# Kernel tuning notes

Measured on AMD Instinct MI355X. Metric: run time of the kernel, lower is better.

The kernel has to match this reference:

```python
import jax, jax.numpy as jnp
import numpy as np

B, N, D, E = 4, 2048, 1024, 4
H = 4 * D  # expert hidden (mult=4)


def setup_inputs() -> dict:
    key = jax.random.key(0)
    ks = jax.random.split(key, 8)
    std = 0.02
    return {
        "x": jax.random.normal(ks[0], (B, N, D), jnp.float32),
        "W_slot": jax.random.normal(ks[1], (E * D, D), jnp.float32) * std,
        "u_slot": jax.random.normal(ks[2], (D,), jnp.float32),
        "sigma_slot": jnp.ones((1,), jnp.float32),
        "W1": jax.random.normal(ks[3], (E, H, D), jnp.float32) * std,
        "b1": jnp.zeros((E, H), jnp.float32),
        "u1": jax.random.normal(ks[4], (E, D), jnp.float32),
        "sig1": jnp.ones((E,), jnp.float32),
        "W2": jax.random.normal(ks[5], (E, D, H), jnp.float32) * std,
        "b2": jnp.zeros((E, D), jnp.float32),
        "u2": jax.random.normal(ks[6], (E, H), jnp.float32),
        "sig2": jnp.ones((E,), jnp.float32),
    }


def _sn_weight(W, u, sigma):
    # One power-iteration step (no_grad in torch -> stop_gradient), then
    # sigma_spec = v^T W u'; weight = W / sigma_spec * learnable sigma.
    v = W @ u
    v = jax.lax.stop_gradient(v / jnp.linalg.norm(v))
    u2 = W.T @ v
    u2 = jax.lax.stop_gradient(u2 / jnp.linalg.norm(u2))
    s = jnp.einsum('c,cd,d->', v, W, u2)
    return W * (sigma / s)


def reference(x, W_slot, u_slot, sigma_slot, W1, b1, u1, sig1, W2, b2, u2, sig2):
    b, n, d = x.shape
    e = W1.shape[0]
    s = n // e  # slots per expert; n divisible by e -> no padding, no mask

    # dynamic slot embeddings from consecutive-segment means
    Wsl = _sn_weight(W_slot, u_slot, sigma_slot[0])          # [e*d, d]
    xm = x.reshape(b, s, e, d).mean(axis=2)                   # [b, s, d]
    slot_embeds = (xm @ Wsl.T).reshape(b, s, e, d)
    slot_embeds = slot_embeds.transpose(0, 2, 1, 3)           # [b, e, s, d]

    logits = jnp.einsum('bnd,besd->bnes', x, slot_embeds)     # [b, n, e, s]
    dispatch = jax.nn.softmax(logits, axis=1)                 # softmax over n
    combine = jax.nn.softmax(logits.reshape(b, n, e * s), axis=-1)

    slots = jnp.einsum('bnd,bnes->ebsd', x, dispatch)         # [e, b, s, d]

    # per-expert FFN with spectral-normed weights (vectorized over experts)
    W1n = jax.vmap(_sn_weight)(W1, u1, sig1)                  # [e, H, d]
    W2n = jax.vmap(_sn_weight)(W2, u2, sig2)                  # [e, d, H]
    h = jax.nn.gelu(jnp.einsum('ebsd,ehd->ebsh', slots, W1n) + b1[:, None, None, :],
                    approximate=False)
    y = jnp.einsum('ebsh,edh->ebsd', h, W2n) + b2[:, None, None, :]

    out = y.transpose(1, 0, 2, 3).reshape(b, e * s, d)        # [b, e*s, d]
    return jnp.einsum('bsd,bns->bnd', out, combine)           # [b, n, d]
```

## Files before the change

kernel.cpp:

```cpp
#include <hip/hip_runtime.h>
#include <hip/hip_bf16.h>
#include <math.h>

constexpr int CB  = 4;
constexpr int CN  = 2048;
constexpr int CD  = 1024;
constexpr int CE  = 4;
constexpr int CS  = 512;
constexpr int CH  = 4096;
constexpr int CES = 2048;

typedef unsigned short u16;
typedef unsigned int   u32;
typedef __bf16 bf16x8 __attribute__((ext_vector_type(8)));
typedef float  f32x4  __attribute__((ext_vector_type(4)));

__device__ __forceinline__ u16 f2bf(float x) {
  u32 u = __float_as_uint(x);
  u = (u + 0x7FFF + ((u >> 16) & 1)) >> 16;
  return (u16)u;
}

__device__ __forceinline__ void gl2lds16(const void* g, void* l) {
  __builtin_amdgcn_global_load_lds(
      (const __attribute__((address_space(1))) void*)g,
      (__attribute__((address_space(3))) void*)l, 16, 0, 0);
}


__global__ __launch_bounds__(256) void gemv_rows_k(const float* __restrict__ W,
    const float* __restrict__ u, float* __restrict__ t1, int M, int K, int ustride) {
  int bi = blockIdx.y;
  int row = blockIdx.x * 4 + (threadIdx.x >> 6);
  int lane = threadIdx.x & 63;
  const float* Wr = W + ((long)bi * M + row) * K;
  const float* ub = u + (long)bi * ustride;
  float s = 0.f;
  for (int k = lane; k < K; k += 64) s += Wr[k] * ub[k];
#pragma unroll
  for (int off = 32; off; off >>= 1) s += __shfl_down(s, off, 64);
  if (lane == 0) t1[bi * M + row] = s;
}

__global__ __launch_bounds__(256) void gemv_cols_k(const float* __restrict__ W,
    const float* __restrict__ t1, float* __restrict__ t2, int M, int K) {
  int bi = blockIdx.z;
  int k = blockIdx.x * 256 + threadIdx.x;
  int m0 = blockIdx.y * 256;
  const float* Wb = W + (long)bi * M * K;
  const float* tb = t1 + bi * M;
  float s = 0.f;
#pragma unroll 4
  for (int m = 0; m < 256; m++) s += Wb[(long)(m0 + m) * K + k] * tb[m0 + m];
  atomicAdd(&t2[bi * K + k], s);
}

__global__ __launch_bounds__(256) void scale_k(const float* __restrict__ t1,
    const float* __restrict__ t2, const float* __restrict__ sig,
    float* __restrict__ out, int M, int K) {
  int bi = blockIdx.x;
  int tid = threadIdx.x;
  __shared__ float red[256];
  float s1 = 0.f;
  for (int i = tid; i < M; i += 256) { float v = t1[bi * M + i]; s1 += v * v; }
  red[tid] = s1; __syncthreads();
  for (int w = 128; w; w >>= 1) { if (tid < w) red[tid] += red[tid + w]; __syncthreads(); }
  float n1 = red[0]; __syncthreads();
  float s2 = 0.f;
  for (int i = tid; i < K; i += 256) { float v = t2[bi * K + i]; s2 += v * v; }
  red[tid] = s2; __syncthreads();
  for (int w = 128; w; w >>= 1) { if (tid < w) red[tid] += red[tid + w]; __syncthreads(); }
  if (tid == 0) out[bi] = sig[bi] * sqrtf(n1 / red[0]);
}

__global__ __launch_bounds__(256) void xm_split_k(const float* __restrict__ x,
    u16* __restrict__ hi, u16* __restrict__ lo) {
  int idx = blockIdx.x * 256 + threadIdx.x;
  int d  = idx & (CD - 1);
  int si = (idx >> 10) & (CS - 1);
  int b  = idx >> 19;
  const float* xp = x + ((long)(b * CN + si * 4)) * CD + d;
  float v = 0.25f * (xp[0] + xp[CD] + xp[2 * CD] + xp[3 * CD]);
  u16 h = f2bf(v);
  hi[idx] = h;
  lo[idx] = f2bf(v - __uint_as_float((u32)h << 16));
}

__global__ __launch_bounds__(256) void split_k(const float* __restrict__ in,
    u16* __restrict__ hi, u16* __restrict__ lo) {
  long i = ((long)blockIdx.x * 256 + threadIdx.x) * 8;
  float4 a = *(const float4*)(in + i);
  float4 b = *(const float4*)(in + i + 4);
  float v[8] = {a.x, a.y, a.z, a.w, b.x, b.y, b.z, b.w};
  u16 oh[8], ol[8];
#pragma unroll
  for (int c = 0; c < 8; c++) {
    u16 h = f2bf(v[c]);
    oh[c] = h;
    ol[c] = f2bf(v[c] - __uint_as_float((u32)h << 16));
  }
  *(uint4*)(hi + i) = *(const uint4*)oh;
  *(uint4*)(lo + i) = *(const uint4*)ol;
}

__global__ __launch_bounds__(256) void colstat_part_k(const float* __restrict__ lg,
    float* __restrict__ pmax, float* __restrict__ psum) {
  int es = blockIdx.x * 256 + threadIdx.x;
  int sl = blockIdx.y;
  int b  = blockIdx.z;
  const float* p = lg + ((long)(b * CN + sl * 256)) * CES + es;
  float m = -1e30f, s = 0.f;
  for (int i = 0; i < 256; i++) {
    float v = p[(long)i * CES];
    if (v > m) { s *= __expf(m - v); m = v; }
    s += __expf(v - m);
  }
  int o = (b * 8 + sl) * CES + es;
  pmax[o] = m; psum[o] = s;
}

__global__ __launch_bounds__(256) void colstat_comb_k(const float* __restrict__ pmax,
    const float* __restrict__ psum, float* __restrict__ cmax, float* __restrict__ csum) {
  int idx = blockIdx.x * 256 + threadIdx.x;
  int b = idx >> 11;
  int es = idx & (CES - 1);
  float m = -1e30f;
#pragma unroll
  for (int sl = 0; sl < 8; sl++) m = fmaxf(m, pmax[(b * 8 + sl) * CES + es]);
  float s = 0.f;
#pragma unroll
  for (int sl = 0; sl < 8; sl++)
    s += psum[(b * 8 + sl) * CES + es] * __expf(pmax[(b * 8 + sl) * CES + es] - m);
  cmax[idx] = m; csum[idx] = s;
}

__global__ __launch_bounds__(256) void rowstat_k(const float* __restrict__ lg,
    float* __restrict__ rmax, float* __restrict__ rsum) {
  int gw = (blockIdx.x * 256 + threadIdx.x) >> 6;
  int lane = threadIdx.x & 63;
  const float* p = lg + (long)gw * CES + lane;
  float v[32];
#pragma unroll
  for (int i = 0; i < 32; i++) v[i] = p[i * 64];
  float m = -1e30f;
#pragma unroll
  for (int i = 0; i < 32; i++) m = fmaxf(m, v[i]);
#pragma unroll
  for (int off = 32; off; off >>= 1) m = fmaxf(m, __shfl_xor(m, off, 64));
  float s = 0.f;
#pragma unroll
  for (int i = 0; i < 32; i++) s += __expf(v[i] - m);
#pragma unroll
  for (int off = 32; off; off >>= 1) s += __shfl_xor(s, off, 64);
  if (lane == 0) { rmax[gw] = m; rsum[gw] = s; }
}

__global__ __launch_bounds__(256) void cvt_bf16_k(const float* __restrict__ in,
                                                  u16* __restrict__ out) {
  long i = ((long)blockIdx.x * 256 + threadIdx.x) * 8;
  float4 a = *(const float4*)(in + i);
  float4 b = *(const float4*)(in + i + 4);
  u16 o[8] = {f2bf(a.x), f2bf(a.y), f2bf(a.z), f2bf(a.w),
              f2bf(b.x), f2bf(b.y), f2bf(b.z), f2bf(b.w)};
  *(uint4*)(out + i) = *(const uint4*)o;
}

__global__ __launch_bounds__(256) void tr_f2b_k(const float* __restrict__ in,
    u16* __restrict__ out, const float* __restrict__ sub, int R, int C, int expmode) {
  __shared__ u16 t[32][33];
  int z = blockIdx.z;
  long ibase = (long)z * R * C;
  int r0 = blockIdx.y * 32, c0 = blockIdx.x * 32;
  int tx = threadIdx.x & 31, ty = threadIdx.x >> 5;
  float cm = expmode ? sub[(long)z * C + c0 + tx] : 0.f;
  for (int rr = ty; rr < 32; rr += 8) {
    float v = in[ibase + (long)(r0 + rr) * C + c0 + tx];
    if (expmode) v = __expf(v - cm);
    t[tx][rr] = f2bf(v);
  }
  __syncthreads();
  for (int cc = ty; cc < 32; cc += 8)
    out[ibase + (long)(c0 + cc) * R + r0 + tx] = t[cc][tx];
}

__global__ __launch_bounds__(256) void tr_b2b_k(const u16* __restrict__ in,
                                                u16* __restrict__ out, int R, int C) {
  __shared__ u16 t[32][33];
  int z = blockIdx.z;
  long ibase = (long)z * R * C;
  int r0 = blockIdx.y * 32, c0 = blockIdx.x * 32;
  int tx = threadIdx.x & 31, ty = threadIdx.x >> 5;
  for (int rr = ty; rr < 32; rr += 8)
    t[tx][rr] = in[ibase + (long)(r0 + rr) * C + c0 + tx];
  __syncthreads();
  for (int cc = ty; cc < 32; cc += 8)
    out[ibase + (long)(c0 + cc) * R + r0 + tx] = t[cc][tx];
}

__global__ __launch_bounds__(256) void combine_k(const float* __restrict__ lg,
    const float* __restrict__ rmax, const float* __restrict__ rsum,
    u16* __restrict__ out) {
  long i = ((long)blockIdx.x * 256 + threadIdx.x) * 8;
  long row = i >> 11;
  float m = rmax[row], inv = 1.f / rsum[row];
  float4 a = *(const float4*)(lg + i);
  float4 b = *(const float4*)(lg + i + 4);
  u16 o[8] = {f2bf(__expf(a.x - m) * inv), f2bf(__expf(a.y - m) * inv),
              f2bf(__expf(a.z - m) * inv), f2bf(__expf(a.w - m) * inv),
              f2bf(__expf(b.x - m) * inv), f2bf(__expf(b.y - m) * inv),
              f2bf(__expf(b.z - m) * inv), f2bf(__expf(b.w - m) * inv)};
  *(uint4*)(out + i) = *(const uint4*)o;
}


struct Ptr3 { const u16* p[3]; };

struct MEpSESplit {
  u16* hi; u16* lo; const float* scale;
  __device__ void store(int z, int m, int n, float v) const {
    v *= scale[0];
    int b = m >> 9, si = m & 511, ei = n >> 10, di = n & 1023;
    long o = ((long)(b * CES + ei * 512 + si)) * CD + di;
    u16 h = f2bf(v);
    hi[o] = h;
    lo[o] = f2bf(v - __uint_as_float((u32)h << 16));
  }
};
struct MEpLogits {
  float* lg;
  __device__ void store(int b, int m, int n, float v) const {
    lg[((long)(b * CN + m)) * CES + n] = v;
  }
};
struct MEpSlots {
  u16* sb; const float* __restrict__ csum;
  __device__ void store(int b, int m, int n, float v) const {
    float inv = 1.f / csum[b * CES + m];
    int e = m >> 9, si = m & 511;
    sb[((long)(e * 2048 + b * 512 + si)) * CD + n] = f2bf(v * inv);
  }
};
struct MEpGelu {
  u16* h; const float* __restrict__ scales; const float* __restrict__ b1;
  __device__ void store(int e, int m, int n, float v) const {
    float xg = v * scales[1 + e] + b1[e * CH + n];
    float g = 0.5f * xg * (1.f + erff(xg * 0.70710678118654752f));
    h[((long)(e * 2048 + m)) * CH + n] = f2bf(g);
  }
};
struct MEpY {
  u16* ob; const float* __restrict__ scales; const float* __restrict__ b2;
  __device__ void store(int e, int m, int n, float v) const {
    int b = m >> 9, si = m & 511;
    ob[((long)(b * CES + e * 512 + si)) * CD + n] = f2bf(v * scales[5 + e] + b2[e * CD + n]);
  }
};
struct MEpOut {
  float* o;
  __device__ void store(int b, int m, int n, float v) const {
    o[((long)(b * CN + m)) * CD + n] = v;
  }
};

template <int NBLK, class EP>
__global__ __launch_bounds__(256) void mgemm_k(Ptr3 A, long Azs, int ldA,
                                               Ptr3 B, long Bzs, int ldB,
                                               EP ep, int KB) {
  constexpr int BM = 128, BN = 128, BK = 32;
  __shared__ __align__(16) u16 As[BM * BK];
  __shared__ __align__(16) u16 Bs[BN * BK];
  const int tid = threadIdx.x;
  const int wid = tid >> 6, lane = tid & 63;
  const int m0 = blockIdx.y * BM, n0 = blockIdx.x * BN;
  const int z = blockIdx.z;
  const int wr = wid >> 1, wc = wid & 1;
  const int srow = lane >> 2;
  const int sk8  = (lane & 3) * 8;

  f32x4 acc[4][4];
  f32x4 zero = {0.f, 0.f, 0.f, 0.f};
#pragma unroll
  for (int i = 0; i < 4; i++)
#pragma unroll
    for (int j = 0; j < 4; j++) acc[i][j] = zero;

  for (int kb = 0; kb < NBLK; kb++) {
    const u16* Az = A.p[kb] + (long)z * Azs;
    const u16* Bz = B.p[kb] + (long)z * Bzs;
    for (int k0 = 0; k0 < KB; k0 += BK) {
#pragma unroll
      for (int i = 0; i < 2; i++) {
        int chunk = i * 4 + wid;
        int r = chunk * 16 + srow;
        gl2lds16(Az + (long)(m0 + r) * ldA + k0 + sk8, (char*)As + chunk * 1024);
        gl2lds16(Bz + (long)(n0 + r) * ldB + k0 + sk8, (char*)Bs + chunk * 1024);
      }
      __syncthreads();
      bf16x8 af[4], bfr[4];
#pragma unroll
      for (int i = 0; i < 4; i++) {
        int arow = wr * 64 + i * 16 + (lane & 15);
        af[i] = *(const bf16x8*)&As[arow * BK + (lane >> 4) * 8];
        int brow = wc * 64 + i * 16 + (lane & 15);
        bfr[i] = *(const bf16x8*)&Bs[brow * BK + (lane >> 4) * 8];
      }
#pragma unroll
      for (int i = 0; i < 4; i++)
#pragma unroll
        for (int j = 0; j < 4; j++)
          acc[i][j] = __builtin_amdgcn_mfma_f32_16x16x32_bf16(af[i], bfr[j], acc[i][j], 0, 0, 0);
      __syncthreads();
    }
  }
#pragma unroll
  for (int i = 0; i < 4; i++) {
    int grow = m0 + wr * 64 + i * 16 + (lane >> 4) * 4;
#pragma unroll
    for (int j = 0; j < 4; j++) {
      int gcol = n0 + wc * 64 + j * 16 + (lane & 15);
#pragma unroll
      for (int r = 0; r < 4; r++)
        ep.store(z, grow + r, gcol, acc[i][j][r]);
    }
  }
}

extern "C" void kernel_launch(void* const* d_in, const int* in_sizes, int n_in,
                              void* d_out, int out_size, void* d_ws, size_t ws_size,
                              hipStream_t stream) {
  const float* x          = (const float*)d_in[0];
  const float* W_slot     = (const float*)d_in[1];
  const float* u_slot     = (const float*)d_in[2];
  const float* sigma_slot = (const float*)d_in[3];
  const float* W1         = (const float*)d_in[4];
  const float* b1         = (const float*)d_in[5];
  const float* u1         = (const float*)d_in[6];
  const float* sig1       = (const float*)d_in[7];
  const float* W2         = (const float*)d_in[8];
  const float* b2         = (const float*)d_in[9];
  const float* u2         = (const float*)d_in[10];
  const float* sig2       = (const float*)d_in[11];
  float* out = (float*)d_out;

  char* ws = (char*)d_ws;
  size_t off = 0;
  auto alloc = [&](size_t bytes) -> char* {
    char* p = ws + off;
    off += (bytes + 255) & ~(size_t)255;
    return p;
  };
  float* t1s = (float*)alloc(4096 * 4);
  float* t1a = (float*)alloc(4 * 4096 * 4);
  float* t1b = (float*)alloc(4 * 1024 * 4);
  float* t2s = (float*)alloc(1024 * 4);
  float* t2a = (float*)alloc(4 * 1024 * 4);
  float* t2b = (float*)alloc(4 * 4096 * 4);
  float* scales = (float*)alloc(16 * 4);
  float* pmax   = (float*)alloc((size_t)CB * 8 * CES * 4);
  float* psum   = (float*)alloc((size_t)CB * 8 * CES * 4);
  float* cmax   = (float*)alloc((size_t)CB * CES * 4);
  float* csum   = (float*)alloc((size_t)CB * CES * 4);
  float* rmax   = (float*)alloc((size_t)CB * CN * 4);
  float* rsum   = (float*)alloc((size_t)CB * CN * 4);
  char* regAB   = alloc((size_t)CB * CN * CD * 2 * 2);
  char* regBB   = alloc((size_t)CB * CES * CD * 2 * 2);
  char* regL    = alloc((size_t)CB * CN * CES * 4);
  char* regS    = alloc((size_t)CE * CB * CS * CD * 2);
  u16* W1b      = (u16*)alloc((size_t)CE * CH * CD * 2);
  u16* W2b      = (u16*)alloc((size_t)CE * CD * CH * 2);

  u16*   xh      = (u16*)regAB;
  u16*   xl      = (u16*)(regAB + (size_t)CB * CN * CD * 2);
  u16*   dispT   = (u16*)regAB;
  u16*   combineB= (u16*)regAB;
  u16*   seh     = (u16*)regBB;
  u16*   sel     = (u16*)(regBB + (size_t)CB * CES * CD * 2);
  u16*   xT      = (u16*)regBB;
  u16*   outbufB = (u16*)(regBB + (size_t)CB * CES * CD * 2);
  float* logits  = (float*)regL;
  u16*   hbuf    = (u16*)regL;
  u16*   xmh     = (u16*)regL;
  u16*   xml     = (u16*)(regL + (size_t)CB * CS * CD * 2);
  u16*   wslh    = (u16*)(regL + (size_t)2 * CB * CS * CD * 2);
  u16*   wsll    = (u16*)(regL + (size_t)2 * CB * CS * CD * 2 + (size_t)CE * CD * CD * 2);
  u16*   slotsB  = (u16*)regS;
  u16*   outbufT = (u16*)regS;

  hipMemsetAsync(t2s, 0, 1024 * 4, stream);
  hipMemsetAsync(t2a, 0, 4 * 1024 * 4, stream);
  hipMemsetAsync(t2b, 0, 4 * 4096 * 4, stream);

  gemv_rows_k<<<dim3(4096 / 4, 1), 256, 0, stream>>>(W_slot, u_slot, t1s, 4096, 1024, 0);
  gemv_rows_k<<<dim3(4096 / 4, 4), 256, 0, stream>>>(W1, u1, t1a, CH, CD, CD);
  gemv_rows_k<<<dim3(1024 / 4, 4), 256, 0, stream>>>(W2, u2, t1b, CD, CH, CH);
  gemv_cols_k<<<dim3(1024 / 256, 4096 / 256, 1), 256, 0, stream>>>(W_slot, t1s, t2s, 4096, 1024);
  gemv_cols_k<<<dim3(1024 / 256, 4096 / 256, 4), 256, 0, stream>>>(W1, t1a, t2a, CH, CD);
  gemv_cols_k<<<dim3(4096 / 256, 1024 / 256, 4), 256, 0, stream>>>(W2, t1b, t2b, CD, CH);
  scale_k<<<1, 256, 0, stream>>>(t1s, t2s, sigma_slot, scales + 0, 4096, 1024);
  scale_k<<<4, 256, 0, stream>>>(t1a, t2a, sig1, scales + 1, CH, CD);
  scale_k<<<4, 256, 0, stream>>>(t1b, t2b, sig2, scales + 5, CD, CH);

  split_k<<<(int)((size_t)CB * CN * CD / 8 / 256), 256, 0, stream>>>(x, xh, xl);
  split_k<<<(int)((size_t)CE * CD * CD / 8 / 256), 256, 0, stream>>>(W_slot, wslh, wsll);
  xm_split_k<<<(CB * CS * CD) / 256, 256, 0, stream>>>(x, xmh, xml);
  cvt_bf16_k<<<(int)((size_t)CE * CH * CD / 8 / 256), 256, 0, stream>>>(W1, W1b);
  cvt_bf16_k<<<(int)((size_t)CE * CD * CH / 8 / 256), 256, 0, stream>>>(W2, W2b);

  mgemm_k<3><<<dim3(4096 / 128, 2048 / 128, 1), 256, 0, stream>>>(
      Ptr3{xmh, xml, xmh}, 0L, CD, Ptr3{wslh, wslh, wsll}, 0L, CD,
      MEpSESplit{seh, sel, scales}, CD);

  mgemm_k<3><<<dim3(CES / 128, CN / 128, CB), 256, 0, stream>>>(
      Ptr3{xh, xl, xh}, (long)CN * CD, CD, Ptr3{seh, seh, sel}, (long)CES * CD, CD,
      MEpLogits{logits}, CD);

  colstat_part_k<<<dim3(CES / 256, 8, CB), 256, 0, stream>>>(logits, pmax, psum);
  colstat_comb_k<<<(CB * CES) / 256, 256, 0, stream>>>(pmax, psum, cmax, csum);

  rowstat_k<<<(CB * CN * 64) / 256, 256, 0, stream>>>(logits, rmax, rsum);

  tr_f2b_k<<<dim3(CES / 32, CN / 32, CB), 256, 0, stream>>>(logits, dispT, cmax, CN, CES, 1);
  tr_f2b_k<<<dim3(CD / 32, CN / 32, CB), 256, 0, stream>>>(x, xT, nullptr, CN, CD, 0);

  mgemm_k<1><<<dim3(CD / 128, CES / 128, CB), 256, 0, stream>>>(
      Ptr3{dispT, dispT, dispT}, (long)CES * CN, CN,
      Ptr3{xT, xT, xT}, (long)CD * CN, CN, MEpSlots{slotsB, csum}, CN);

  combine_k<<<(int)((size_t)CB * CN * CES / 8 / 256), 256, 0, stream>>>(logits, rmax, rsum, combineB);

  mgemm_k<1><<<dim3(CH / 128, 2048 / 128, CE), 256, 0, stream>>>(
      Ptr3{slotsB, slotsB, slotsB}, (long)2048 * CD, CD,
      Ptr3{W1b, W1b, W1b}, (long)CH * CD, CD, MEpGelu{hbuf, scales, b1}, CD);

  mgemm_k<1><<<dim3(CD / 128, 2048 / 128, CE), 256, 0, stream>>>(
      Ptr3{hbuf, hbuf, hbuf}, (long)2048 * CH, CH,
      Ptr3{W2b, W2b, W2b}, (long)CD * CH, CH, MEpY{outbufB, scales, b2}, CH);

  tr_b2b_k<<<dim3(CD / 32, CES / 32, CB), 256, 0, stream>>>(outbufB, outbufT, CES, CD);

  mgemm_k<1><<<dim3(CD / 128, CN / 128, CB), 256, 0, stream>>>(
      Ptr3{combineB, combineB, combineB}, (long)CN * CES, CES,
      Ptr3{outbufT, outbufT, outbufT}, (long)CD * CES, CES, MEpOut{out}, CES);

  (void)in_sizes; (void)n_in; (void)out_size; (void)ws_size;
}
```

Before: 957.0 us.

## Fuse weight bf16 conversion into gemv, fuse row softmax, add XCD swizzle and 3-term GEMM

The weight-to-bf16 (and hi/lo split) conversion now happens inside the column power-iteration GEMV, which already reads the weights, so the separate conversion kernels and their extra weight reads go away. The rowstat and combine kernels are merged into one block-per-row softmax kernel. GEMM launches get an XCD-aware block remap to improve L2 locality. The three-pass split-precision GEMM becomes a single K loop that loads hi/lo tiles once and issues three MFMAs per step. The costs are uncoalesced 2-byte stores in the GEMV and more LDS per block in the fused split GEMM.

```diff
diff --git a/kernel.cpp b/kernel.cpp
--- a/kernel.cpp
+++ b/kernel.cpp
@@ -25,6 +25,18 @@
   __builtin_amdgcn_global_load_lds(
       (const __attribute__((address_space(1))) void*)g,
       (__attribute__((address_space(3))) void*)l, 16, 0, 0);
+}
+
+__device__ __forceinline__ void xcd_swz(int& bx, int& by, int& bz) {
+  u32 gx = gridDim.x, gy = gridDim.y;
+  u32 w = blockIdx.x + gx * (blockIdx.y + gy * blockIdx.z);
+  u32 nwg = gx * gy * gridDim.z;
+  u32 q = nwg >> 3;
+  u32 wg = (w & 7) * q + (w >> 3);
+  bx = wg % gx;
+  u32 r = wg / gx;
+  by = r % gy;
+  bz = r / gy;
 }
 
 
@@ -43,15 +55,25 @@
 }
 
 __global__ __launch_bounds__(256) void gemv_cols_k(const float* __restrict__ W,
-    const float* __restrict__ t1, float* __restrict__ t2, int M, int K) {
+    const float* __restrict__ t1, float* __restrict__ t2,
+    u16* __restrict__ bh, u16* __restrict__ bl, int M, int K) {
   int bi = blockIdx.z;
   int k = blockIdx.x * 256 + threadIdx.x;
   int m0 = blockIdx.y * 256;
   const float* Wb = W + (long)bi * M * K;
   const float* tb = t1 + bi * M;
+  u16* bhb = bh + (long)bi * M * K;
+  u16* blb = bl ? bl + (long)bi * M * K : nullptr;
   float s = 0.f;
 #pragma unroll 4
-  for (int m = 0; m < 256; m++) s += Wb[(long)(m0 + m) * K + k] * tb[m0 + m];
+  for (int m = 0; m < 256; m++) {
+    long idx = (long)(m0 + m) * K + k;
+    float w = Wb[idx];
+    s += w * tb[m0 + m];
+    u16 h = f2bf(w);
+    bhb[idx] = h;
+    if (blb) blb[idx] = f2bf(w - __uint_as_float((u32)h << 16));
+  }
   atomicAdd(&t2[bi * K + k], s);
 }
 
@@ -134,35 +156,35 @@
   cmax[idx] = m; csum[idx] = s;
 }
 
-__global__ __launch_bounds__(256) void rowstat_k(const float* __restrict__ lg,
-    float* __restrict__ rmax, float* __restrict__ rsum) {
-  int gw = (blockIdx.x * 256 + threadIdx.x) >> 6;
-  int lane = threadIdx.x & 63;
-  const float* p = lg + (long)gw * CES + lane;
-  float v[32];
-#pragma unroll
-  for (int i = 0; i < 32; i++) v[i] = p[i * 64];
-  float m = -1e30f;
-#pragma unroll
-  for (int i = 0; i < 32; i++) m = fmaxf(m, v[i]);
+__global__ __launch_bounds__(256) void rowcomb_k(const float* __restrict__ lg,
+                                                 u16* __restrict__ outB) {
+  __shared__ float red[8];
+  long row = blockIdx.x;
+  const float* p = lg + row * CES + threadIdx.x * 8;
+  float4 a = *(const float4*)p;
+  float4 b = *(const float4*)(p + 4);
+  float v[8] = {a.x, a.y, a.z, a.w, b.x, b.y, b.z, b.w};
+  float m = v[0];
+#pragma unroll
+  for (int c = 1; c < 8; c++) m = fmaxf(m, v[c]);
 #pragma unroll
   for (int off = 32; off; off >>= 1) m = fmaxf(m, __shfl_xor(m, off, 64));
+  int wv = threadIdx.x >> 6;
+  if ((threadIdx.x & 63) == 0) red[wv] = m;
+  __syncthreads();
+  m = fmaxf(fmaxf(red[0], red[1]), fmaxf(red[2], red[3]));
   float s = 0.f;
 #pragma unroll
-  for (int i = 0; i < 32; i++) s += __expf(v[i] - m);
+  for (int c = 0; c < 8; c++) { v[c] = __expf(v[c] - m); s += v[c]; }
 #pragma unroll
   for (int off = 32; off; off >>= 1) s += __shfl_xor(s, off, 64);
-  if (lane == 0) { rmax[gw] = m; rsum[gw] = s; }
-}
-
-__global__ __launch_bounds__(256) void cvt_bf16_k(const float* __restrict__ in,
-                                                  u16* __restrict__ out) {
-  long i = ((long)blockIdx.x * 256 + threadIdx.x) * 8;
-  float4 a = *(const float4*)(in + i);
-  float4 b = *(const float4*)(in + i + 4);
-  u16 o[8] = {f2bf(a.x), f2bf(a.y), f2bf(a.z), f2bf(a.w),
-              f2bf(b.x), f2bf(b.y), f2bf(b.z), f2bf(b.w)};
-  *(uint4*)(out + i) = *(const uint4*)o;
+  if ((threadIdx.x & 63) == 0) red[4 + wv] = s;
+  __syncthreads();
+  float inv = 1.f / (red[4] + red[5] + red[6] + red[7]);
+  u16 o[8];
+#pragma unroll
+  for (int c = 0; c < 8; c++) o[c] = f2bf(v[c] * inv);
+  *(uint4*)(outB + row * CES + threadIdx.x * 8) = *(const uint4*)o;
 }
 
 __global__ __launch_bounds__(256) void tr_f2b_k(const float* __restrict__ in,
@@ -197,24 +219,6 @@
     out[ibase + (long)(c0 + cc) * R + r0 + tx] = t[cc][tx];
 }
 
-__global__ __launch_bounds__(256) void combine_k(const float* __restrict__ lg,
-    const float* __restrict__ rmax, const float* __restrict__ rsum,
-    u16* __restrict__ out) {
-  long i = ((long)blockIdx.x * 256 + threadIdx.x) * 8;
-  long row = i >> 11;
-  float m = rmax[row], inv = 1.f / rsum[row];
-  float4 a = *(const float4*)(lg + i);
-  float4 b = *(const float4*)(lg + i + 4);
-  u16 o[8] = {f2bf(__expf(a.x - m) * inv), f2bf(__expf(a.y - m) * inv),
-              f2bf(__expf(a.z - m) * inv), f2bf(__expf(a.w - m) * inv),
-              f2bf(__expf(b.x - m) * inv), f2bf(__expf(b.y - m) * inv),
-              f2bf(__expf(b.z - m) * inv), f2bf(__expf(b.w - m) * inv)};
-  *(uint4*)(out + i) = *(const uint4*)o;
-}
-
-
-struct Ptr3 { const u16* p[3]; };
-
 struct MEpSESplit {
   u16* hi; u16* lo; const float* scale;
   __device__ void store(int z, int m, int n, float v) const {
@@ -262,17 +266,21 @@
   }
 };
 
-template <int NBLK, class EP>
-__global__ __launch_bounds__(256) void mgemm_k(Ptr3 A, long Azs, int ldA,
-                                               Ptr3 B, long Bzs, int ldB,
-                                               EP ep, int KB) {
-  constexpr int BM = 128, BN = 128, BK = 32;
-  __shared__ __align__(16) u16 As[BM * BK];
-  __shared__ __align__(16) u16 Bs[BN * BK];
+
+template <class EP>
+__global__ __launch_bounds__(256) void mgemm_k(const u16* __restrict__ A, long Azs, int ldA,
+                                               const u16* __restrict__ B, long Bzs, int ldB,
+                                               EP ep, int K) {
+  constexpr int BK = 32;
+  __shared__ __align__(16) u16 As[128 * BK];
+  __shared__ __align__(16) u16 Bs[128 * BK];
+  int bx, by, bz;
+  xcd_swz(bx, by, bz);
   const int tid = threadIdx.x;
   const int wid = tid >> 6, lane = tid & 63;
-  const int m0 = blockIdx.y * BM, n0 = blockIdx.x * BN;
-  const int z = blockIdx.z;
+  const int m0 = by * 128, n0 = bx * 128;
+  const u16* Az = A + (long)bz * Azs;
+  const u16* Bz = B + (long)bz * Bzs;
   const int wr = wid >> 1, wc = wid & 1;
   const int srow = lane >> 2;
   const int sk8  = (lane & 3) * 8;
@@ -284,33 +292,29 @@
 #pragma unroll
     for (int j = 0; j < 4; j++) acc[i][j] = zero;
 
-  for (int kb = 0; kb < NBLK; kb++) {
-    const u16* Az = A.p[kb] + (long)z * Azs;
-    const u16* Bz = B.p[kb] + (long)z * Bzs;
-    for (int k0 = 0; k0 < KB; k0 += BK) {
-#pragma unroll
-      for (int i = 0; i < 2; i++) {
-        int chunk = i * 4 + wid;
-        int r = chunk * 16 + srow;
-        gl2lds16(Az + (long)(m0 + r) * ldA + k0 + sk8, (char*)As + chunk * 1024);
-        gl2lds16(Bz + (long)(n0 + r) * ldB + k0 + sk8, (char*)Bs + chunk * 1024);
-      }
-      __syncthreads();
-      bf16x8 af[4], bfr[4];
-#pragma unroll
-      for (int i = 0; i < 4; i++) {
-        int arow = wr * 64 + i * 16 + (lane & 15);
-        af[i] = *(const bf16x8*)&As[arow * BK + (lane >> 4) * 8];
-        int brow = wc * 64 + i * 16 + (lane & 15);
-        bfr[i] = *(const bf16x8*)&Bs[brow * BK + (lane >> 4) * 8];
-      }
-#pragma unroll
-      for (int i = 0; i < 4; i++)
-#pragma unroll
-        for (int j = 0; j < 4; j++)
-          acc[i][j] = __builtin_amdgcn_mfma_f32_16x16x32_bf16(af[i], bfr[j], acc[i][j], 0, 0, 0);
-      __syncthreads();
+  for (int k0 = 0; k0 < K; k0 += BK) {
+#pragma unroll
+    for (int i = 0; i < 2; i++) {
+      int chunk = i * 4 + wid;
+      int r = chunk * 16 + srow;
+      gl2lds16(Az + (long)(m0 + r) * ldA + k0 + sk8, (char*)As + chunk * 1024);
+      gl2lds16(Bz + (long)(n0 + r) * ldB + k0 + sk8, (char*)Bs + chunk * 1024);
     }
+    __syncthreads();
+    bf16x8 af[4], bfr[4];
+#pragma unroll
+    for (int i = 0; i < 4; i++) {
+      int arow = wr * 64 + i * 16 + (lane & 15);
+      af[i] = *(const bf16x8*)&As[arow * BK + (lane >> 4) * 8];
+      int brow = wc * 64 + i * 16 + (lane & 15);
+      bfr[i] = *(const bf16x8*)&Bs[brow * BK + (lane >> 4) * 8];
+    }
+#pragma unroll
+    for (int i = 0; i < 4; i++)
+#pragma unroll
+      for (int j = 0; j < 4; j++)
+        acc[i][j] = __builtin_amdgcn_mfma_f32_16x16x32_bf16(af[i], bfr[j], acc[i][j], 0, 0, 0);
+    __syncthreads();
   }
 #pragma unroll
   for (int i = 0; i < 4; i++) {
@@ -320,7 +324,86 @@
       int gcol = n0 + wc * 64 + j * 16 + (lane & 15);
 #pragma unroll
       for (int r = 0; r < 4; r++)
-        ep.store(z, grow + r, gcol, acc[i][j][r]);
+        ep.store(bz, grow + r, gcol, acc[i][j][r]);
+    }
+  }
+}
+
+template <class EP>
+__global__ __launch_bounds__(256) void mgemm3_k(const u16* __restrict__ Ah,
+                                                const u16* __restrict__ Al, long Azs, int ldA,
+                                                const u16* __restrict__ Bh,
+                                                const u16* __restrict__ Bl, long Bzs, int ldB,
+                                                EP ep, int K) {
+  constexpr int BK = 32;
+  __shared__ __align__(16) u16 Ahs[128 * BK];
+  __shared__ __align__(16) u16 Als[128 * BK];
+  __shared__ __align__(16) u16 Bhs[128 * BK];
+  __shared__ __align__(16) u16 Bls[128 * BK];
+  int bx, by, bz;
+  xcd_swz(bx, by, bz);
+  const int tid = threadIdx.x;
+  const int wid = tid >> 6, lane = tid & 63;
+  const int m0 = by * 128, n0 = bx * 128;
+  const u16* Ahz = Ah + (long)bz * Azs;
+  const u16* Alz = Al + (long)bz * Azs;
+  const u16* Bhz = Bh + (long)bz * Bzs;
+  const u16* Blz = Bl + (long)bz * Bzs;
+  const int wr = wid >> 1, wc = wid & 1;
+  const int srow = lane >> 2;
+  const int sk8  = (lane & 3) * 8;
+
+  f32x4 acc[4][4];
+  f32x4 zero = {0.f, 0.f, 0.f, 0.f};
+#pragma unroll
+  for (int i = 0; i < 4; i++)
+#pragma unroll
+    for (int j = 0; j < 4; j++) acc[i][j] = zero;
+
+  for (int k0 = 0; k0 < K; k0 += BK) {
+#pragma unroll
+    for (int i = 0; i < 2; i++) {
+      int chunk = i * 4 + wid;
+      int r = chunk * 16 + srow;
+      long ao = (long)(m0 + r) * ldA + k0 + sk8;
+      long bo = (long)(n0 + r) * ldB + k0 + sk8;
+      gl2lds16(Ahz + ao, (char*)Ahs + chunk * 1024);
+      gl2lds16(Alz + ao, (char*)Als + chunk * 1024);
+      gl2lds16(Bhz + bo, (char*)Bhs + chunk * 1024);
+      gl2lds16(Blz + bo, (char*)Bls + chunk * 1024);
+    }
+    __syncthreads();
+    bf16x8 ah[4], al[4], bh[4], bl[4];
+#pragma unroll
+    for (int i = 0; i < 4; i++) {
+      int arow = wr * 64 + i * 16 + (lane & 15);
+      int aoff = arow * BK + (lane >> 4) * 8;
+      ah[i] = *(const bf16x8*)&Ahs[aoff];
+      al[i] = *(const bf16x8*)&Als[aoff];
+      int brow = wc * 64 + i * 16 + (lane & 15);
+      int boff = brow * BK + (lane >> 4) * 8;
+      bh[i] = *(const bf16x8*)&Bhs[boff];
+      bl[i] = *(const bf16x8*)&Bls[boff];
+    }
+#pragma unroll
+    for (int i = 0; i < 4; i++)
+#pragma unroll
+      for (int j = 0; j < 4; j++) {
+        acc[i][j] = __builtin_amdgcn_mfma_f32_16x16x32_bf16(ah[i], bh[j], acc[i][j], 0, 0, 0);
+        acc[i][j] = __builtin_amdgcn_mfma_f32_16x16x32_bf16(al[i], bh[j], acc[i][j], 0, 0, 0);
+        acc[i][j] = __builtin_amdgcn_mfma_f32_16x16x32_bf16(ah[i], bl[j], acc[i][j], 0, 0, 0);
+      }
+    __syncthreads();
+  }
+#pragma unroll
+  for (int i = 0; i < 4; i++) {
+    int grow = m0 + wr * 64 + i * 16 + (lane >> 4) * 4;
+#pragma unroll
+    for (int j = 0; j < 4; j++) {
+      int gcol = n0 + wc * 64 + j * 16 + (lane & 15);
+#pragma unroll
+      for (int r = 0; r < 4; r++)
+        ep.store(bz, grow + r, gcol, acc[i][j][r]);
     }
   }
 }
@@ -360,8 +443,6 @@
   float* psum   = (float*)alloc((size_t)CB * 8 * CES * 4);
   float* cmax   = (float*)alloc((size_t)CB * CES * 4);
   float* csum   = (float*)alloc((size_t)CB * CES * 4);
-  float* rmax   = (float*)alloc((size_t)CB * CN * 4);
-  float* rsum   = (float*)alloc((size_t)CB * CN * 4);
   char* regAB   = alloc((size_t)CB * CN * CD * 2 * 2);
   char* regBB   = alloc((size_t)CB * CES * CD * 2 * 2);
   char* regL    = alloc((size_t)CB * CN * CES * 4);
@@ -393,54 +474,44 @@
   gemv_rows_k<<<dim3(4096 / 4, 1), 256, 0, stream>>>(W_slot, u_slot, t1s, 4096, 1024, 0);
   gemv_rows_k<<<dim3(4096 / 4, 4), 256, 0, stream>>>(W1, u1, t1a, CH, CD, CD);
   gemv_rows_k<<<dim3(1024 / 4, 4), 256, 0, stream>>>(W2, u2, t1b, CD, CH, CH);
-  gemv_cols_k<<<dim3(1024 / 256, 4096 / 256, 1), 256, 0, stream>>>(W_slot, t1s, t2s, 4096, 1024);
-  gemv_cols_k<<<dim3(1024 / 256, 4096 / 256, 4), 256, 0, stream>>>(W1, t1a, t2a, CH, CD);
-  gemv_cols_k<<<dim3(4096 / 256, 1024 / 256, 4), 256, 0, stream>>>(W2, t1b, t2b, CD, CH);
+  gemv_cols_k<<<dim3(1024 / 256, 4096 / 256, 1), 256, 0, stream>>>(W_slot, t1s, t2s, wslh, wsll, 4096, 1024);
+  gemv_cols_k<<<dim3(1024 / 256, 4096 / 256, 4), 256, 0, stream>>>(W1, t1a, t2a, W1b, nullptr, CH, CD);
+  gemv_cols_k<<<dim3(4096 / 256, 1024 / 256, 4), 256, 0, stream>>>(W2, t1b, t2b, W2b, nullptr, CD, CH);
   scale_k<<<1, 256, 0, stream>>>(t1s, t2s, sigma_slot, scales + 0, 4096, 1024);
   scale_k<<<4, 256, 0, stream>>>(t1a, t2a, sig1, scales + 1, CH, CD);
   scale_k<<<4, 256, 0, stream>>>(t1b, t2b, sig2, scales + 5, CD, CH);
 
   split_k<<<(int)((size_t)CB * CN * CD / 8 / 256), 256, 0, stream>>>(x, xh, xl);
-  split_k<<<(int)((size_t)CE * CD * CD / 8 / 256), 256, 0, stream>>>(W_slot, wslh, wsll);
   xm_split_k<<<(CB * CS * CD) / 256, 256, 0, stream>>>(x, xmh, xml);
-  cvt_bf16_k<<<(int)((size_t)CE * CH * CD / 8 / 256), 256, 0, stream>>>(W1, W1b);
-  cvt_bf16_k<<<(int)((size_t)CE * CD * CH / 8 / 256), 256, 0, stream>>>(W2, W2b);
-
-  mgemm_k<3><<<dim3(4096 / 128, 2048 / 128, 1), 256, 0, stream>>>(
-      Ptr3{xmh, xml, xmh}, 0L, CD, Ptr3{wslh, wslh, wsll}, 0L, CD,
-      MEpSESplit{seh, sel, scales}, CD);
-
-  mgemm_k<3><<<dim3(CES / 128, CN / 128, CB), 256, 0, stream>>>(
-      Ptr3{xh, xl, xh}, (long)CN * CD, CD, Ptr3{seh, seh, sel}, (long)CES * CD, CD,
+
+  mgemm3_k<<<dim3(4096 / 128, 2048 / 128, 1), 256, 0, stream>>>(
+      xmh, xml, 0L, CD, wslh, wsll, 0L, CD, MEpSESplit{seh, sel, scales}, CD);
+
+  mgemm3_k<<<dim3(CES / 128, CN / 128, CB), 256, 0, stream>>>(
+      xh, xl, (long)CN * CD, CD, seh, sel, (long)CES * CD, CD,
       MEpLogits{logits}, CD);
 
   colstat_part_k<<<dim3(CES / 256, 8, CB), 256, 0, stream>>>(logits, pmax, psum);
   colstat_comb_k<<<(CB * CES) / 256, 256, 0, stream>>>(pmax, psum, cmax, csum);
 
-  rowstat_k<<<(CB * CN * 64) / 256, 256, 0, stream>>>(logits, rmax, rsum);
-
   tr_f2b_k<<<dim3(CES / 32, CN / 32, CB), 256, 0, stream>>>(logits, dispT, cmax, CN, CES, 1);
   tr_f2b_k<<<dim3(CD / 32, CN / 32, CB), 256, 0, stream>>>(x, xT, nullptr, CN, CD, 0);
 
-  mgemm_k<1><<<dim3(CD / 128, CES / 128, CB), 256, 0, stream>>>(
-      Ptr3{dispT, dispT, dispT}, (long)CES * CN, CN,
-      Ptr3{xT, xT, xT}, (long)CD * CN, CN, MEpSlots{slotsB, csum}, CN);
-
-  combine_k<<<(int)((size_t)CB * CN * CES / 8 / 256), 256, 0, stream>>>(logits, rmax, rsum, combineB);
-
-  mgemm_k<1><<<dim3(CH / 128, 2048 / 128, CE), 256, 0, stream>>>(
-      Ptr3{slotsB, slotsB, slotsB}, (long)2048 * CD, CD,
-      Ptr3{W1b, W1b, W1b}, (long)CH * CD, CD, MEpGelu{hbuf, scales, b1}, CD);
-
-  mgemm_k<1><<<dim3(CD / 128, 2048 / 128, CE), 256, 0, stream>>>(
-      Ptr3{hbuf, hbuf, hbuf}, (long)2048 * CH, CH,
-      Ptr3{W2b, W2b, W2b}, (long)CD * CH, CH, MEpY{outbufB, scales, b2}, CH);
+  mgemm_k<<<dim3(CD / 128, CES / 128, CB), 256, 0, stream>>>(
+      dispT, (long)CES * CN, CN, xT, (long)CD * CN, CN, MEpSlots{slotsB, csum}, CN);
+
+  rowcomb_k<<<CB * CN, 256, 0, stream>>>(logits, combineB);
+
+  mgemm_k<<<dim3(CH / 128, 2048 / 128, CE), 256, 0, stream>>>(
+      slotsB, (long)2048 * CD, CD, W1b, (long)CH * CD, CD, MEpGelu{hbuf, scales, b1}, CD);
+
+  mgemm_k<<<dim3(CD / 128, 2048 / 128, CE), 256, 0, stream>>>(
+      hbuf, (long)2048 * CH, CH, W2b, (long)CD * CH, CH, MEpY{outbufB, scales, b2}, CH);
 
   tr_b2b_k<<<dim3(CD / 32, CES / 32, CB), 256, 0, stream>>>(outbufB, outbufT, CES, CD);
 
-  mgemm_k<1><<<dim3(CD / 128, CN / 128, CB), 256, 0, stream>>>(
-      Ptr3{combineB, combineB, combineB}, (long)CN * CES, CES,
-      Ptr3{outbufT, outbufT, outbufT}, (long)CD * CES, CES, MEpOut{out}, CES);
+  mgemm_k<<<dim3(CD / 128, CN / 128, CB), 256, 0, stream>>>(
+      combineB, (long)CN * CES, CES, outbufT, (long)CD * CES, CES, MEpOut{out}, CES);
 
   (void)in_sizes; (void)n_in; (void)out_size; (void)ws_size;
 }
```

New measurement: 924.3 us. -3.4%, faster.
